# Kernel optimization log

Measured on AMD Instinct MI355X. Metric: run time of the kernel, lower is better.

Reference implementation:

```python
import jax, jax.numpy as jnp
import numpy as np

EPS_BN = 1e-5
HEADS = 4
K = 16

def _bn_eval(x, g, b, m, v):
    # eval-mode BatchNorm1d over the feature (last) axis
    return (x - m) * (g / jnp.sqrt(v + EPS_BN)) + b

def setup_inputs() -> dict:
    key = jax.random.key(0)
    ks = jax.random.split(key, 32)
    B, T, N, C = 8, 4, 2048, 11
    D = 64
    hd = D // HEADS
    s = 0.05
    rn = lambda k, shp: jax.random.normal(k, shp, jnp.float32) * s
    inp = {
        'x': jax.random.normal(ks[0], (B, T, N, C), jnp.float32),
        # PointEmbedding: Linear(11,32) + BN(32) + ReLU + Linear(32,64) + BN(64) + ReLU
        'emb_w1': rn(ks[1], (32, C)), 'emb_b1': rn(ks[2], (32,)),
        'bn1_g': jnp.ones((32,)), 'bn1_b': jnp.zeros((32,)),
        'bn1_m': rn(ks[3], (32,)), 'bn1_v': jnp.ones((32,)),
        'emb_w2': rn(ks[4], (D, 32)), 'emb_b2': rn(ks[5], (D,)),
        'bn2_g': jnp.ones((D,)), 'bn2_b': jnp.zeros((D,)),
        'bn2_m': rn(ks[6], (D,)), 'bn2_v': jnp.ones((D,)),
        # DenseGATLayer
        'gat_W': rn(ks[7], (D, D)),          # Linear(64,64,bias=False)
        'att': rn(ks[8], (HEADS, 2 * hd)),    # attention vector per head
        # TemporalCrossAttention
        'q_w': rn(ks[9], (D, D)), 'q_b': rn(ks[10], (D,)),
        'kv_w': rn(ks[11], (D, D)), 'kv_b': rn(ks[12], (D,)),
        # heads
        'lw1': rn(ks[13], (32, D)), 'lb1': rn(ks[14], (32,)),
        'lw2': rn(ks[15], (4, 32)), 'lb2': rn(ks[16], (4,)),
        'rw1': rn(ks[17], (32, D)), 'rb1': rn(ks[18], (32,)),
        'rw2': rn(ks[19], (4, 32)), 'rb2': rn(ks[20], (4,)),
    }
    return inp

def _forward(x, emb_w1, emb_b1, bn1_g, bn1_b, bn1_m, bn1_v,
             emb_w2, emb_b2, bn2_g, bn2_b, bn2_m, bn2_v,
             gat_W, att, q_w, q_b, kv_w, kv_b,
             lw1, lb1, lw2, lb2, rw1, rb1, rw2, rb2):
    B, T, N, C = x.shape
    D = gat_W.shape[0]
    hd = D // HEADS
    BT = B * T
    xf = x.reshape(BT, N, C)

    # ---- PointEmbedding (BN in eval mode) ----
    h = xf @ emb_w1.T + emb_b1
    h = jax.nn.relu(_bn_eval(h, bn1_g, bn1_b, bn1_m, bn1_v))
    h = h @ emb_w2.T + emb_b2
    h = jax.nn.relu(_bn_eval(h, bn2_g, bn2_b, bn2_m, bn2_v))  # [BT,N,D]

    # ---- DenseGATLayer ----
    pos = xf[:, :, :2]  # raw xy
    sq = jnp.sum(pos * pos, axis=-1)  # [BT,N]
    d2 = sq[:, :, None] + sq[:, None, :] - 2.0 * jnp.einsum('bnc,bmc->bnm', pos, pos)
    _, idx = jax.lax.top_k(-d2, K)  # k nearest (incl self), [BT,N,K]

    hw = (h @ gat_W.T).reshape(BT, N, HEADS, hd)  # [BT,N,H,hd]
    h_nb = jax.vmap(lambda hb, ib: hb[ib])(hw, idx)  # [BT,N,K,H,hd]

    att_self, att_nb = att[:, :hd], att[:, hd:]
    s_self = jnp.einsum('bnhd,hd->bnh', hw, att_self)       # [BT,N,H]
    s_nb = jnp.einsum('bnkhd,hd->bnkh', h_nb, att_nb)        # [BT,N,K,H]
    scores = jax.nn.leaky_relu(s_self[:, :, None, :] + s_nb, 0.2)
    alpha = jax.nn.softmax(scores, axis=2)                   # softmax over K
    out = jnp.einsum('bnkhd,bnkh->bnhd', h_nb, alpha).reshape(BT, N, D)
    h_sp = jax.nn.relu(out + h)  # [BT,N,D]

    # ---- TemporalCrossAttention ----
    ht = h_sp.reshape(B, T, N, D).transpose(0, 2, 1, 3)  # [B,N,T,D]
    Q = ht[:, :, -1, :] @ q_w.T + q_b                    # [B,N,D]
    KV = ht @ kv_w.T + kv_b                              # [B,N,T,D]
    sc = jnp.einsum('bnd,bntd->bnt', Q, KV) / jnp.sqrt(jnp.float32(D))
    w = jax.nn.softmax(sc, axis=-1)
    h_fused = jnp.einsum('bnt,bntd->bnd', w, KV)         # [B,N,D]

    # ---- heads ----
    ol = jax.nn.relu(h_fused @ lw1.T + lb1) @ lw2.T + lb2
    orr = jax.nn.relu(h_fused @ rw1.T + rb1) @ rw2.T + rb2
    lidar_mu, lidar_sigma = ol[:, :, :2], jax.nn.softplus(ol[:, :, 2:]) + 1e-6
    radar_mu, radar_sigma = orr[:, :, :2], jax.nn.softplus(orr[:, :, 2:]) + 1e-6
    return ((lidar_mu, lidar_sigma), (radar_mu, radar_sigma))

def reference(x, emb_w1, emb_b1, bn1_g, bn1_b, bn1_m, bn1_v,
              emb_w2, emb_b2, bn2_g, bn2_b, bn2_m, bn2_v,
              gat_W, att, q_w, q_b, kv_w, kv_b,
              lw1, lb1, lw2, lb2, rw1, rb1, rw2, rb2):
    return _forward(x, emb_w1, emb_b1, bn1_g, bn1_b, bn1_m, bn1_v,
                    emb_w2, emb_b2, bn2_g, bn2_b, bn2_m, bn2_v,
                    gat_W, att, q_w, q_b, kv_w, kv_b,
                    lw1, lb1, lw2, lb2, rw1, rb1, rw2, rb2)
```

## Files before the change

### kernel.cpp

```cpp
#include <hip/hip_runtime.h>
#include <math.h>

#define B_ 8
#define T_ 4
#define N_ 2048
#define C_ 11
#define D_ 64
#define H_ 4
#define HD_ 16
#define K_ 16
#define BT_ (B_*T_)

__device__ __forceinline__ float softplus_f(float x) {
    return fmaxf(x, 0.f) + log1pf(expf(-fabsf(x)));
}

__global__ __launch_bounds__(1024) void k_sort(const float* __restrict__ x,
    float2* __restrict__ sp2g, int* __restrict__ sidg, int* __restrict__ fail_cnt)
{
    __shared__ unsigned long long kvs[N_];
    __shared__ float lyy[N_];
    int t = threadIdx.x, bt = blockIdx.x;
    if (t == 0) fail_cnt[bt] = 0;
    const float* xb = x + (size_t)bt * N_ * C_;
    for (int m = t; m < N_; m += 1024) {
        float a = xb[m*C_], b = xb[m*C_+1];
        unsigned int bits = __float_as_uint(a);
        unsigned int u = (bits & 0x80000000u) ? ~bits : (bits | 0x80000000u);
        kvs[m] = ((unsigned long long)u << 11) | (unsigned)m;
        lyy[m] = b;
    }
    __syncthreads();
    for (int k = 2; k <= N_; k <<= 1) {
        for (int j = k >> 1; j > 0; j >>= 1) {
            int p = t;
            int i = ((p & ~(j-1)) << 1) | (p & (j-1));
            int l = i | j;
            unsigned long long a = kvs[i], b = kvs[l];
            bool asc = (i & k) == 0;
            if ((a > b) == asc) { kvs[i] = b; kvs[l] = a; }
            __syncthreads();
        }
    }
    float2* op = sp2g + (size_t)bt * N_;
    int*    oi = sidg + (size_t)bt * N_;
    for (int m = t; m < N_; m += 1024) {
        unsigned long long key = kvs[m];
        int id = (int)(key & 0x7FFull);
        unsigned int u = (unsigned int)(key >> 11);
        unsigned int bits = (u & 0x80000000u) ? (u & 0x7FFFFFFFu) : ~u;
        op[m] = make_float2(__uint_as_float(bits), lyy[id]);
        oi[m] = id;
    }
}

__global__ __launch_bounds__(256) void k_embed(
    const float* __restrict__ x,
    const float* __restrict__ w1, const float* __restrict__ b1,
    const float* __restrict__ g1, const float* __restrict__ bb1,
    const float* __restrict__ m1, const float* __restrict__ v1,
    const float* __restrict__ w2, const float* __restrict__ b2,
    const float* __restrict__ g2, const float* __restrict__ bb2,
    const float* __restrict__ m2, const float* __restrict__ v2,
    float* __restrict__ h)
{
    __shared__ float sw1[32*C_], sb1[32], sw2[D_*32], sb2[D_];
    int t = threadIdx.x;
    if (t < 32) {
        float s = g1[t] / sqrtf(v1[t] + 1e-5f);
        sb1[t] = (b1[t] - m1[t]) * s + bb1[t];
        for (int c = 0; c < C_; ++c) sw1[t*C_+c] = w1[t*C_+c] * s;
    } else if (t >= 64 && t < 128) {
        int j = t - 64;
        float s = g2[j] / sqrtf(v2[j] + 1e-5f);
        sb2[j] = (b2[j] - m2[j]) * s + bb2[j];
        int key = (j >> 4) & 3;
        for (int c = 0; c < 32; ++c)
            sw2[j*32 + ((((c>>2) ^ key) << 2) | (c & 3))] = w2[j*32+c] * s;
    }
    __syncthreads();

    int node = blockIdx.x * 64 + (t >> 2);
    int g = t & 3;
    const float* xp = x + (size_t)node * C_;
    float xin[C_];
    #pragma unroll
    for (int c = 0; c < C_; ++c) xin[c] = xp[c];

    float t1[32];
    #pragma unroll
    for (int j = 0; j < 32; ++j) {
        float a = sb1[j];
        #pragma unroll
        for (int c = 0; c < C_; ++c) a = fmaf(xin[c], sw1[j*C_+c], a);
        t1[j] = fmaxf(a, 0.f);
    }
    float4* hp4 = (float4*)(h + (size_t)node * D_ + g * 16);
    #pragma unroll
    for (int j4 = 0; j4 < 4; ++j4) {
        float o[4];
        #pragma unroll
        for (int u = 0; u < 4; ++u) {
            int j = g*16 + j4*4 + u;
            float a = sb2[j];
            #pragma unroll
            for (int c4 = 0; c4 < 8; ++c4) {
                float4 w4 = *(const float4*)(&sw2[j*32 + ((c4 ^ g) << 2)]);
                a = fmaf(t1[4*c4+0], w4.x, a);
                a = fmaf(t1[4*c4+1], w4.y, a);
                a = fmaf(t1[4*c4+2], w4.z, a);
                a = fmaf(t1[4*c4+3], w4.w, a);
            }
            o[u] = fmaxf(a, 0.f);
        }
        hp4[j4] = make_float4(o[0], o[1], o[2], o[3]);
    }
}

__global__ __launch_bounds__(256) void k_gatw(
    const float* __restrict__ h, const float* __restrict__ gw,
    const float* __restrict__ att,
    float* __restrict__ hw, float* __restrict__ ssf, float* __restrict__ snbf)
{
    __shared__ float sw[D_*D_];
    __shared__ float satA[2*H_*HD_];
    int t = threadIdx.x;
    for (int i = t; i < D_*D_; i += 256) {
        int r = i >> 6, c = i & 63;
        sw[r*64 + ((((c>>2) ^ ((r>>4)&3)) << 2) | (c & 3))] = gw[i];
    }
    if (t < 2*H_*HD_) satA[t] = att[t];
    __syncthreads();

    int node = blockIdx.x * 64 + (t >> 2);
    int hh = t & 3;
    const float* hp = h + (size_t)node * D_;
    float hin[D_];
    #pragma unroll
    for (int j = 0; j < D_; j += 4) {
        float4 v = *(const float4*)(hp + j);
        hin[j] = v.x; hin[j+1] = v.y; hin[j+2] = v.z; hin[j+3] = v.w;
    }
    float4* wp4 = (float4*)(hw + (size_t)node * D_ + hh * HD_);
    float ss = 0.f, sn = 0.f;
    #pragma unroll
    for (int q4 = 0; q4 < 4; ++q4) {
        float o[4];
        #pragma unroll
        for (int u = 0; u < 4; ++u) {
            const int jj = q4*4 + u;
            const int j = hh*HD_ + jj;
            float a = 0.f;
            #pragma unroll
            for (int c4 = 0; c4 < D_/4; ++c4) {
                float4 w4 = *(const float4*)(&sw[j*64 + ((c4 ^ hh) << 2)]);
                a = fmaf(hin[4*c4+0], w4.x, a);
                a = fmaf(hin[4*c4+1], w4.y, a);
                a = fmaf(hin[4*c4+2], w4.z, a);
                a = fmaf(hin[4*c4+3], w4.w, a);
            }
            o[u] = a;
            ss = fmaf(a, satA[hh*(2*HD_) + jj], ss);
            sn = fmaf(a, satA[hh*(2*HD_) + HD_ + jj], sn);
        }
        wp4[q4] = make_float4(o[0], o[1], o[2], o[3]);
    }
    ssf[(size_t)node * H_ + hh] = ss;
    snbf[(size_t)node * H_ + hh] = sn;
}

__global__ __launch_bounds__(256) void k_knn_b1(const float2* __restrict__ sp2g,
    const int* __restrict__ sidg, int* __restrict__ idx,
    int* __restrict__ fail_cnt, int* __restrict__ fail_lst)
{
    __shared__ float2 spw[640];
    __shared__ int sidw[640];
    __shared__ int scnt[64];
    const int bt    = blockIdx.x >> 5;
    const int qbase = (blockIdx.x & 31) << 6;
    const int base  = qbase - 288;
    const float2* pb = sp2g + (size_t)bt * N_;
    const int*    ib = sidg + (size_t)bt * N_;
    for (int L = threadIdx.x; L < 640; L += 256) {
        int r = base + L;
        if (r < 0 || r >= N_) { spw[L] = make_float2(1e18f, 0.f); sidw[L] = 0; }
        else { spw[L] = pb[r]; sidw[L] = ib[r]; }
    }
    if (threadIdx.x < 64) scnt[threadIdx.x] = 0;
    __syncthreads();

    const int q = threadIdx.x >> 2;
    const int g = threadIdx.x & 3;
    const int s = qbase + q;
    const int sLoc = q + 288;
    const float xs = spw[sLoc].x, ys = spw[sLoc].y;
    const float sqn = __fmaf_rn(xs, xs, __fmul_rn(ys, ys));

    float bd[K_];
    #pragma unroll
    for (int i = 0; i < K_; ++i) bd[i] = 3.402823466e38f;

    for (int i = 0; i < 8; ++i) {
        float d[16];
        #pragma unroll
        for (int j = 0; j < 16; ++j) {
            float2 p = spw[q + 32 + 64*i + 4*j + g];
            float sps = __fmaf_rn(p.x, p.x, __fmul_rn(p.y, p.y));
            float tt = __fmul_rn(xs, p.x);
            tt = __fmaf_rn(ys, p.y, tt);
            d[j] = __fmaf_rn(-2.f, tt, sps);
        }
        #pragma unroll
        for (int k = 2; k <= 16; k <<= 1) {
            #pragma unroll
            for (int jj = k >> 1; jj > 0; jj >>= 1) {
                #pragma unroll
                for (int ii = 0; ii < 16; ++ii) {
                    int ll = ii ^ jj;
                    if (ll > ii) {
                        float lo = fminf(d[ii], d[ll]);
                        float hi = fmaxf(d[ii], d[ll]);
                        if ((ii & k) == 0) { d[ii] = lo; d[ll] = hi; }
                        else               { d[ii] = hi; d[ll] = lo; }
                    }
                }
            }
        }
        #pragma unroll
        for (int ii = 0; ii < 16; ++ii) bd[ii] = fminf(bd[ii], d[15-ii]);
        #pragma unroll
        for (int jj = 8; jj > 0; jj >>= 1) {
            #pragma unroll
            for (int ii = 0; ii < 16; ++ii) {
                int ll = ii ^ jj;
                if (ll > ii) {
                    float lo = fminf(bd[ii], bd[ll]);
                    float hi = fmaxf(bd[ii], bd[ll]);
                    bd[ii] = lo; bd[ll] = hi;
                }
            }
        }
    }

    #pragma unroll
    for (int st = 1; st <= 2; st <<= 1) {
        float pr[K_];
        #pragma unroll
        for (int i = 0; i < K_; ++i) pr[i] = __shfl_xor(bd[K_-1-i], st, 64);
        #pragma unroll
        for (int i = 0; i < K_; ++i) bd[i] = fminf(bd[i], pr[i]);
        #pragma unroll
        for (int dd = 8; dd >= 1; dd >>= 1) {
            #pragma unroll
            for (int i = 0; i < K_; ++i) {
                if ((i & dd) == 0) {
                    float lo = fminf(bd[i], bd[i+dd]);
                    float hi = fmaxf(bd[i], bd[i+dd]);
                    bd[i] = lo; bd[i+dd] = hi;
                }
            }
        }
    }
    const float d15 = bd[K_-1];

    float d15s = d15 + sqn;
    float bound = d15s * 1.0001f + (sqn + 1.0f) * 1e-5f;
    bool leftOK = (s - 257 < 0);
    if (!leftOK) { float gp = xs - spw[q+31].x;  leftOK  = (gp*gp >= bound); }
    bool rightOK = (s + 256 > N_-1);
    if (!rightOK){ float gp = spw[q+544].x - xs; rightOK = (gp*gp >= bound); }
    if (!(leftOK && rightOK) && g == 0) {
        int fp = atomicAdd(&fail_cnt[bt], 1);
        fail_lst[bt*N_ + fp] = s;
    }

    int n = sidw[sLoc];
    int* op = idx + ((size_t)bt * N_ + n) * K_;
    for (int i = 0; i < 16; ++i) {
        float d[8];
        int Lb = q + 32 + 32*i + g;
        #pragma unroll
        for (int j = 0; j < 8; ++j) {
            float2 p = spw[Lb + 4*j];
            float sps = __fmaf_rn(p.x, p.x, __fmul_rn(p.y, p.y));
            float tt = __fmul_rn(xs, p.x);
            tt = __fmaf_rn(ys, p.y, tt);
            d[j] = __fmaf_rn(-2.f, tt, sps);
        }
        float dm0 = fminf(fminf(d[0],d[1]), fminf(d[2],d[3]));
        float dm1 = fminf(fminf(d[4],d[5]), fminf(d[6],d[7]));
        if (fminf(dm0, dm1) <= d15) {
            #pragma unroll
            for (int j = 0; j < 8; ++j) {
                if (d[j] <= d15) {
                    int c = atomicAdd(&scnt[q], 1);
                    if (c < K_) op[c] = sidw[Lb + 4*j];
                }
            }
        }
    }
}

__global__ __launch_bounds__(256) void k_knn_b2(const float2* __restrict__ sp2g,
    const int* __restrict__ sidg, const int* __restrict__ fail_cnt,
    const int* __restrict__ fail_lst, int* __restrict__ idx)
{
    const int bt    = blockIdx.x >> 7;
    const int chunk = blockIdx.x & 127;
    const int nf = fail_cnt[bt];
    if (chunk * 16 >= nf) return;

    __shared__ float2 sp[N_];
    __shared__ int sid[N_];
    __shared__ int scnt[16];
    const float2* pb = sp2g + (size_t)bt * N_;
    const int*    ib = sidg + (size_t)bt * N_;
    for (int m = threadIdx.x; m < N_; m += 256) { sp[m] = pb[m]; sid[m] = ib[m]; }
    if (threadIdx.x < 16) scnt[threadIdx.x] = 0;
    __syncthreads();

    const int q = threadIdx.x >> 4;
    const int g = threadIdx.x & 15;
    const bool active = (chunk*16 + q) < nf;
    const int s = active ? fail_lst[bt*N_ + chunk*16 + q] : 0;
    const float xs = sp[s].x, ys = sp[s].y;

    float bd[K_];
    #pragma unroll
    for (int i = 0; i < K_; ++i) bd[i] = 3.402823466e38f;

    for (int i = 0; i < 8; ++i) {
        float d[16];
        #pragma unroll
        for (int j = 0; j < 16; ++j) {
            float2 p = sp[256*i + 16*j + g];
            float sps = __fmaf_rn(p.x, p.x, __fmul_rn(p.y, p.y));
            float tt = __fmul_rn(xs, p.x);
            tt = __fmaf_rn(ys, p.y, tt);
            d[j] = __fmaf_rn(-2.f, tt, sps);
        }
        #pragma unroll
        for (int k = 2; k <= 16; k <<= 1) {
            #pragma unroll
            for (int jj = k >> 1; jj > 0; jj >>= 1) {
                #pragma unroll
                for (int ii = 0; ii < 16; ++ii) {
                    int ll = ii ^ jj;
                    if (ll > ii) {
                        float lo = fminf(d[ii], d[ll]);
                        float hi = fmaxf(d[ii], d[ll]);
                        if ((ii & k) == 0) { d[ii] = lo; d[ll] = hi; }
                        else               { d[ii] = hi; d[ll] = lo; }
                    }
                }
            }
        }
        #pragma unroll
        for (int ii = 0; ii < 16; ++ii) bd[ii] = fminf(bd[ii], d[15-ii]);
        #pragma unroll
        for (int jj = 8; jj > 0; jj >>= 1) {
            #pragma unroll
            for (int ii = 0; ii < 16; ++ii) {
                int ll = ii ^ jj;
                if (ll > ii) {
                    float lo = fminf(bd[ii], bd[ll]);
                    float hi = fmaxf(bd[ii], bd[ll]);
                    bd[ii] = lo; bd[ll] = hi;
                }
            }
        }
    }

    #pragma unroll
    for (int st = 1; st <= 8; st <<= 1) {
        float pr[K_];
        #pragma unroll
        for (int i = 0; i < K_; ++i) pr[i] = __shfl_xor(bd[K_-1-i], st, 64);
        #pragma unroll
        for (int i = 0; i < K_; ++i) bd[i] = fminf(bd[i], pr[i]);
        #pragma unroll
        for (int dd = 8; dd >= 1; dd >>= 1) {
            #pragma unroll
            for (int i = 0; i < K_; ++i) {
                if ((i & dd) == 0) {
                    float lo = fminf(bd[i], bd[i+dd]);
                    float hi = fmaxf(bd[i], bd[i+dd]);
                    bd[i] = lo; bd[i+dd] = hi;
                }
            }
        }
    }
    const float d15 = bd[K_-1];

    int n = sid[s];
    int* op = idx + ((size_t)bt * N_ + n) * K_;
    for (int i = 0; i < 16; ++i) {
        float d[8];
        #pragma unroll
        for (int j = 0; j < 8; ++j) {
            float2 p = sp[128*i + 16*j + g];
            float sps = __fmaf_rn(p.x, p.x, __fmul_rn(p.y, p.y));
            float tt = __fmul_rn(xs, p.x);
            tt = __fmaf_rn(ys, p.y, tt);
            d[j] = __fmaf_rn(-2.f, tt, sps);
        }
        float dm0 = fminf(fminf(d[0],d[1]), fminf(d[2],d[3]));
        float dm1 = fminf(fminf(d[4],d[5]), fminf(d[6],d[7]));
        if (active && fminf(dm0, dm1) <= d15) {
            #pragma unroll
            for (int j = 0; j < 8; ++j) {
                if (d[j] <= d15) {
                    int c = atomicAdd(&scnt[q], 1);
                    if (c < K_) op[c] = sid[128*i + 16*j + g];
                }
            }
        }
    }
}

__global__ __launch_bounds__(256, 4) void k_gat(
    const float* __restrict__ hw, const float* __restrict__ ssf,
    const float* __restrict__ snbf,
    const int* __restrict__ idx,
    float* __restrict__ h )
{
    const int t = threadIdx.x;
    const int xcd   = blockIdx.x & 7;
    const int local = blockIdx.x >> 3;
    const int btl   = local >> 5;
    const int chunk = local & 31;
    const int bt    = xcd * 4 + btl;
    const int node  = bt * N_ + chunk * 64 + (t >> 2);
    const int hh    = t & 3;

    const int* ip = idx + (size_t)node * K_;
    float ssv = ssf[(size_t)node*H_ + hh];
    const float* hwb = hw + ((size_t)bt * N_) * D_;
    const float* snb = snbf + ((size_t)bt * N_) * H_;

    int nb[K_];
    #pragma unroll
    for (int k = 0; k < K_; ++k) nb[k] = ip[k];

    float sc[K_];
    float mx = -3.402823466e38f;
    #pragma unroll
    for (int k = 0; k < K_; ++k) {
        float s = ssv + snb[(size_t)nb[k]*H_ + hh];
        s = (s >= 0.f) ? s : 0.2f * s;
        sc[k] = s;
        mx = fmaxf(mx, s);
    }
    float den = 0.f;
    #pragma unroll
    for (int k = 0; k < K_; ++k) { sc[k] = __expf(sc[k] - mx); den += sc[k]; }
    float inv = 1.f / den;

    float acc[HD_];
    #pragma unroll
    for (int i = 0; i < HD_; ++i) acc[i] = 0.f;
    #pragma unroll
    for (int k = 0; k < K_; ++k) {
        float al = sc[k] * inv;
        const float* vp = hwb + (size_t)nb[k]*D_ + hh*HD_;
        #pragma unroll
        for (int i = 0; i < HD_; i += 4) {
            float4 v = *(const float4*)(vp + i);
            acc[i]   = fmaf(v.x, al, acc[i]);
            acc[i+1] = fmaf(v.y, al, acc[i+1]);
            acc[i+2] = fmaf(v.z, al, acc[i+2]);
            acc[i+3] = fmaf(v.w, al, acc[i+3]);
        }
    }
    float4* hp4 = (float4*)(h + (size_t)node*D_ + hh*HD_);
    #pragma unroll
    for (int i4 = 0; i4 < 4; ++i4) {
        float4 old = hp4[i4];
        hp4[i4] = make_float4(fmaxf(acc[4*i4+0] + old.x, 0.f),
                              fmaxf(acc[4*i4+1] + old.y, 0.f),
                              fmaxf(acc[4*i4+2] + old.z, 0.f),
                              fmaxf(acc[4*i4+3] + old.w, 0.f));
    }
}

__global__ __launch_bounds__(256) void k_qkv(
    const float* __restrict__ hsp,
    const float* __restrict__ qw, const float* __restrict__ qb,
    const float* __restrict__ kw, const float* __restrict__ kb,
    float* __restrict__ q, float* __restrict__ kv)
{
    __shared__ float s_qw[D_*D_], s_kw[D_*D_], s_qb[D_], s_kb[D_];
    int t = threadIdx.x;
    for (int i = t; i < D_*D_; i += 256) {
        int r = i >> 6, c = i & 63;
        int p = r*64 + ((((c>>2) ^ ((r>>4)&3)) << 2) | (c & 3));
        s_qw[p] = qw[i]; s_kw[p] = kw[i];
    }
    if (t < D_) { s_qb[t] = qb[t]; s_kb[t] = kb[t]; }
    __syncthreads();

    int r = blockIdx.x * 64 + (t >> 2);
    int g = t & 3;
    const float* in; float* outp; const float* W; const float* bb;
    if (r < BT_*N_) {
        int bt = r >> 11; int n = r & (N_-1);
        int b = bt >> 2, tt = bt & 3;
        in = hsp + (size_t)r * D_;
        outp = kv + (((size_t)(b*N_ + n))*T_ + tt) * D_;
        W = s_kw; bb = s_kb;
    } else {
        int rr = r - BT_*N_;
        int b = rr >> 11, n = rr & (N_-1);
        in = hsp + ((size_t)(b*T_ + (T_-1))*N_ + n) * D_;
        outp = q + (size_t)rr * D_;
        W = s_qw; bb = s_qb;
    }
    float xin[D_];
    #pragma unroll
    for (int j = 0; j < D_; j += 4) {
        float4 v = *(const float4*)(in + j);
        xin[j] = v.x; xin[j+1] = v.y; xin[j+2] = v.z; xin[j+3] = v.w;
    }
    float4* outp4 = (float4*)(outp + g * 16);
    #pragma unroll
    for (int j4 = 0; j4 < 4; ++j4) {
        float o[4];
        #pragma unroll
        for (int u = 0; u < 4; ++u) {
            int j = g*16 + j4*4 + u;
            float a = bb[j];
            #pragma unroll
            for (int c4 = 0; c4 < D_/4; ++c4) {
                float4 w4 = *(const float4*)(&W[j*64 + ((c4 ^ g) << 2)]);
                a = fmaf(xin[4*c4+0], w4.x, a);
                a = fmaf(xin[4*c4+1], w4.y, a);
                a = fmaf(xin[4*c4+2], w4.z, a);
                a = fmaf(xin[4*c4+3], w4.w, a);
            }
            o[u] = a;
        }
        outp4[j4] = make_float4(o[0], o[1], o[2], o[3]);
    }
}

__global__ __launch_bounds__(64) void k_head(
    const float* __restrict__ q, const float* __restrict__ kv,
    const float* __restrict__ lw1, const float* __restrict__ lb1,
    const float* __restrict__ lw2, const float* __restrict__ lb2,
    const float* __restrict__ rw1, const float* __restrict__ rb1,
    const float* __restrict__ rw2, const float* __restrict__ rb2,
    float* __restrict__ out)
{
    __shared__ float sl1[32*D_], sr1[32*D_], sl2[4*32], sr2[4*32];
    __shared__ float slb1[32], srb1[32], slb2[4], srb2[4];
    int t = threadIdx.x;
    for (int i = t; i < 32*D_; i += 64) { sl1[i] = lw1[i]; sr1[i] = rw1[i]; }
    for (int i = t; i < 128; i += 64)   { sl2[i] = lw2[i]; sr2[i] = rw2[i]; }
    if (t < 32) { slb1[t] = lb1[t]; srb1[t] = rb1[t]; }
    if (t < 4)  { slb2[t] = lb2[t]; srb2[t] = rb2[t]; }
    __syncthreads();

    int rn = blockIdx.x * 64 + t;
    const float* qp = q + (size_t)rn * D_;
    const float* kp = kv + (size_t)rn * T_ * D_;

    float qv[D_];
    #pragma unroll
    for (int j = 0; j < D_; j += 4) {
        float4 v = *(const float4*)(qp + j);
        qv[j] = v.x; qv[j+1] = v.y; qv[j+2] = v.z; qv[j+3] = v.w;
    }
    float scv[T_];
    #pragma unroll
    for (int tt = 0; tt < T_; ++tt) {
        float a = 0.f;
        const float4* kr = (const float4*)(kp + tt*D_);
        #pragma unroll
        for (int c4 = 0; c4 < D_/4; ++c4) {
            float4 v = kr[c4];
            a = fmaf(qv[4*c4+0], v.x, a);
            a = fmaf(qv[4*c4+1], v.y, a);
            a = fmaf(qv[4*c4+2], v.z, a);
            a = fmaf(qv[4*c4+3], v.w, a);
        }
        scv[tt] = a * 0.125f;
    }
    float mx = fmaxf(fmaxf(scv[0], scv[1]), fmaxf(scv[2], scv[3]));
    float wsum = 0.f;
    #pragma unroll
    for (int tt = 0; tt < T_; ++tt) { scv[tt] = expf(scv[tt] - mx); wsum += scv[tt]; }
    float winv = 1.f / wsum;

    float hf[D_];
    #pragma unroll
    for (int j = 0; j < D_; ++j) hf[j] = 0.f;
    #pragma unroll
    for (int tt = 0; tt < T_; ++tt) {
        float w = scv[tt] * winv;
        const float4* kr = (const float4*)(kp + tt*D_);
        #pragma unroll
        for (int c4 = 0; c4 < D_/4; ++c4) {
            float4 v = kr[c4];
            hf[4*c4+0] = fmaf(v.x, w, hf[4*c4+0]);
            hf[4*c4+1] = fmaf(v.y, w, hf[4*c4+1]);
            hf[4*c4+2] = fmaf(v.z, w, hf[4*c4+2]);
            hf[4*c4+3] = fmaf(v.w, w, hf[4*c4+3]);
        }
    }
    float ol0 = slb2[0], ol1 = slb2[1], ol2 = slb2[2], ol3 = slb2[3];
    #pragma unroll 2
    for (int j = 0; j < 32; ++j) {
        float a = slb1[j];
        const float4* wr = (const float4*)(&sl1[j*D_]);
        #pragma unroll
        for (int c4 = 0; c4 < D_/4; ++c4) {
            float4 v = wr[c4];
            a = fmaf(hf[4*c4+0], v.x, a);
            a = fmaf(hf[4*c4+1], v.y, a);
            a = fmaf(hf[4*c4+2], v.z, a);
            a = fmaf(hf[4*c4+3], v.w, a);
        }
        a = fmaxf(a, 0.f);
        ol0 = fmaf(a, sl2[0*32+j], ol0);
        ol1 = fmaf(a, sl2[1*32+j], ol1);
        ol2 = fmaf(a, sl2[2*32+j], ol2);
        ol3 = fmaf(a, sl2[3*32+j], ol3);
    }
    float or0 = srb2[0], or1 = srb2[1], or2 = srb2[2], or3 = srb2[3];
    #pragma unroll 2
    for (int j = 0; j < 32; ++j) {
        float a = srb1[j];
        const float4* wr = (const float4*)(&sr1[j*D_]);
        #pragma unroll
        for (int c4 = 0; c4 < D_/4; ++c4) {
            float4 v = wr[c4];
            a = fmaf(hf[4*c4+0], v.x, a);
            a = fmaf(hf[4*c4+1], v.y, a);
            a = fmaf(hf[4*c4+2], v.z, a);
            a = fmaf(hf[4*c4+3], v.w, a);
        }
        a = fmaxf(a, 0.f);
        or0 = fmaf(a, sr2[0*32+j], or0);
        or1 = fmaf(a, sr2[1*32+j], or1);
        or2 = fmaf(a, sr2[2*32+j], or2);
        or3 = fmaf(a, sr2[3*32+j], or3);
    }
    const int NB = B_ * N_;
    out[0*2*NB + rn*2 + 0] = ol0;
    out[0*2*NB + rn*2 + 1] = ol1;
    out[1*2*NB + rn*2 + 0] = softplus_f(ol2) + 1e-6f;
    out[1*2*NB + rn*2 + 1] = softplus_f(ol3) + 1e-6f;
    out[2*2*NB + rn*2 + 0] = or0;
    out[2*2*NB + rn*2 + 1] = or1;
    out[3*2*NB + rn*2 + 0] = softplus_f(or2) + 1e-6f;
    out[3*2*NB + rn*2 + 1] = softplus_f(or3) + 1e-6f;
}

extern "C" void kernel_launch(void* const* d_in, const int* in_sizes, int n_in,
                              void* d_out, int out_size, void* d_ws, size_t ws_size,
                              hipStream_t stream)
{
    const float* x   = (const float*)d_in[0];
    const float* ew1 = (const float*)d_in[1];
    const float* eb1 = (const float*)d_in[2];
    const float* g1  = (const float*)d_in[3];
    const float* bb1 = (const float*)d_in[4];
    const float* m1  = (const float*)d_in[5];
    const float* v1  = (const float*)d_in[6];
    const float* ew2 = (const float*)d_in[7];
    const float* eb2 = (const float*)d_in[8];
    const float* g2  = (const float*)d_in[9];
    const float* bb2 = (const float*)d_in[10];
    const float* m2  = (const float*)d_in[11];
    const float* v2  = (const float*)d_in[12];
    const float* gw  = (const float*)d_in[13];
    const float* att = (const float*)d_in[14];
    const float* qw  = (const float*)d_in[15];
    const float* qb  = (const float*)d_in[16];
    const float* kw  = (const float*)d_in[17];
    const float* kb  = (const float*)d_in[18];
    const float* lw1 = (const float*)d_in[19];
    const float* lb1 = (const float*)d_in[20];
    const float* lw2 = (const float*)d_in[21];
    const float* lb2 = (const float*)d_in[22];
    const float* rw1 = (const float*)d_in[23];
    const float* rb1 = (const float*)d_in[24];
    const float* rw2 = (const float*)d_in[25];
    const float* rb2 = (const float*)d_in[26];
    float* out = (float*)d_out;

    const size_t NTOT = (size_t)BT_*N_;
    float* h    = (float*)d_ws;
    float* hw   = h   + NTOT*D_;
    float* kvb  = hw  + NTOT*D_;
    float* ssf  = kvb + NTOT*D_;
    float* snbf = ssf + NTOT*H_;
    int*   idx  = (int*)(snbf + NTOT*H_);
    float* q    = (float*)(idx + NTOT*K_);
    float2* sp2g = (float2*)(q + (size_t)B_*N_*D_);
    int*   sidg = (int*)((float*)sp2g + 2*NTOT);
    int*   fail_cnt = sidg + NTOT;
    int*   fail_lst = fail_cnt + 32;

    k_sort<<<BT_, 1024, 0, stream>>>(x, sp2g, sidg, fail_cnt);
    k_embed<<<BT_*N_/64, 256, 0, stream>>>(x, ew1, eb1, g1, bb1, m1, v1,
                                           ew2, eb2, g2, bb2, m2, v2, h);
    k_gatw<<<BT_*N_/64, 256, 0, stream>>>(h, gw, att, hw, ssf, snbf);
    k_knn_b1<<<BT_*(N_/64), 256, 0, stream>>>(sp2g, sidg, idx, fail_cnt, fail_lst);
    k_knn_b2<<<BT_*128, 256, 0, stream>>>(sp2g, sidg, fail_cnt, fail_lst, idx);
    k_gat<<<(BT_*N_*H_)/256, 256, 0, stream>>>(hw, ssf, snbf, idx, h);
    k_qkv<<<(BT_*N_ + B_*N_)/64, 256, 0, stream>>>(h, qw, qb, kw, kb, q, kvb);
    k_head<<<(B_*N_)/64, 64, 0, stream>>>(q, kvb, lw1, lb1, lw2, lb2,
                                          rw1, rb1, rw2, rb2, out);
}
```

Before: 216.8 us.

## Merge independent kernels into block-partitioned launches to overlap sort/embed and gatw/knn

Result: faster. 210.6 us (median of 3 runs) (-2.8%).

```diff
diff --git a/kernel.cpp b/kernel.cpp
--- a/kernel.cpp
+++ b/kernel.cpp
@@ -15,46 +15,7 @@
     return fmaxf(x, 0.f) + log1pf(expf(-fabsf(x)));
 }
 
-__global__ __launch_bounds__(1024) void k_sort(const float* __restrict__ x,
-    float2* __restrict__ sp2g, int* __restrict__ sidg, int* __restrict__ fail_cnt)
-{
-    __shared__ unsigned long long kvs[N_];
-    __shared__ float lyy[N_];
-    int t = threadIdx.x, bt = blockIdx.x;
-    if (t == 0) fail_cnt[bt] = 0;
-    const float* xb = x + (size_t)bt * N_ * C_;
-    for (int m = t; m < N_; m += 1024) {
-        float a = xb[m*C_], b = xb[m*C_+1];
-        unsigned int bits = __float_as_uint(a);
-        unsigned int u = (bits & 0x80000000u) ? ~bits : (bits | 0x80000000u);
-        kvs[m] = ((unsigned long long)u << 11) | (unsigned)m;
-        lyy[m] = b;
-    }
-    __syncthreads();
-    for (int k = 2; k <= N_; k <<= 1) {
-        for (int j = k >> 1; j > 0; j >>= 1) {
-            int p = t;
-            int i = ((p & ~(j-1)) << 1) | (p & (j-1));
-            int l = i | j;
-            unsigned long long a = kvs[i], b = kvs[l];
-            bool asc = (i & k) == 0;
-            if ((a > b) == asc) { kvs[i] = b; kvs[l] = a; }
-            __syncthreads();
-        }
-    }
-    float2* op = sp2g + (size_t)bt * N_;
-    int*    oi = sidg + (size_t)bt * N_;
-    for (int m = t; m < N_; m += 1024) {
-        unsigned long long key = kvs[m];
-        int id = (int)(key & 0x7FFull);
-        unsigned int u = (unsigned int)(key >> 11);
-        unsigned int bits = (u & 0x80000000u) ? (u & 0x7FFFFFFFu) : ~u;
-        op[m] = make_float2(__uint_as_float(bits), lyy[id]);
-        oi[m] = id;
-    }
-}
-
-__global__ __launch_bounds__(256) void k_embed(
+__global__ __launch_bounds__(1024) void k_root(
     const float* __restrict__ x,
     const float* __restrict__ w1, const float* __restrict__ b1,
     const float* __restrict__ g1, const float* __restrict__ bb1,
@@ -62,135 +23,182 @@
     const float* __restrict__ w2, const float* __restrict__ b2,
     const float* __restrict__ g2, const float* __restrict__ bb2,
     const float* __restrict__ m2, const float* __restrict__ v2,
-    float* __restrict__ h)
+    float* __restrict__ h,
+    float2* __restrict__ sp2g, int* __restrict__ sidg, int* __restrict__ fail_cnt)
 {
-    __shared__ float sw1[32*C_], sb1[32], sw2[D_*32], sb2[D_];
+    __shared__ unsigned long long smemU[3072];
     int t = threadIdx.x;
-    if (t < 32) {
-        float s = g1[t] / sqrtf(v1[t] + 1e-5f);
-        sb1[t] = (b1[t] - m1[t]) * s + bb1[t];
-        for (int c = 0; c < C_; ++c) sw1[t*C_+c] = w1[t*C_+c] * s;
-    } else if (t >= 64 && t < 128) {
-        int j = t - 64;
-        float s = g2[j] / sqrtf(v2[j] + 1e-5f);
-        sb2[j] = (b2[j] - m2[j]) * s + bb2[j];
-        int key = (j >> 4) & 3;
-        for (int c = 0; c < 32; ++c)
-            sw2[j*32 + ((((c>>2) ^ key) << 2) | (c & 3))] = w2[j*32+c] * s;
-    }
-    __syncthreads();
-
-    int node = blockIdx.x * 64 + (t >> 2);
-    int g = t & 3;
-    const float* xp = x + (size_t)node * C_;
-    float xin[C_];
-    #pragma unroll
-    for (int c = 0; c < C_; ++c) xin[c] = xp[c];
-
-    float t1[32];
-    #pragma unroll
-    for (int j = 0; j < 32; ++j) {
-        float a = sb1[j];
-        #pragma unroll
-        for (int c = 0; c < C_; ++c) a = fmaf(xin[c], sw1[j*C_+c], a);
-        t1[j] = fmaxf(a, 0.f);
-    }
-    float4* hp4 = (float4*)(h + (size_t)node * D_ + g * 16);
-    #pragma unroll
-    for (int j4 = 0; j4 < 4; ++j4) {
-        float o[4];
-        #pragma unroll
-        for (int u = 0; u < 4; ++u) {
-            int j = g*16 + j4*4 + u;
-            float a = sb2[j];
-            #pragma unroll
-            for (int c4 = 0; c4 < 8; ++c4) {
-                float4 w4 = *(const float4*)(&sw2[j*32 + ((c4 ^ g) << 2)]);
-                a = fmaf(t1[4*c4+0], w4.x, a);
-                a = fmaf(t1[4*c4+1], w4.y, a);
-                a = fmaf(t1[4*c4+2], w4.z, a);
-                a = fmaf(t1[4*c4+3], w4.w, a);
-            }
-            o[u] = fmaxf(a, 0.f);
-        }
-        hp4[j4] = make_float4(o[0], o[1], o[2], o[3]);
+
+    if (blockIdx.x < BT_) {
+        unsigned long long* kvs = smemU;
+        float* lyy = (float*)(smemU + 2048);
+        int bt = blockIdx.x;
+        if (t == 0) fail_cnt[bt] = 0;
+        const float* xb = x + (size_t)bt * N_ * C_;
+        for (int m = t; m < N_; m += 1024) {
+            float a = xb[m*C_], b = xb[m*C_+1];
+            unsigned int bits = __float_as_uint(a);
+            unsigned int u = (bits & 0x80000000u) ? ~bits : (bits | 0x80000000u);
+            kvs[m] = ((unsigned long long)u << 11) | (unsigned)m;
+            lyy[m] = b;
+        }
+        __syncthreads();
+        for (int k = 2; k <= N_; k <<= 1) {
+            for (int j = k >> 1; j > 0; j >>= 1) {
+                int p = t;
+                int i = ((p & ~(j-1)) << 1) | (p & (j-1));
+                int l = i | j;
+                unsigned long long a = kvs[i], b = kvs[l];
+                bool asc = (i & k) == 0;
+                if ((a > b) == asc) { kvs[i] = b; kvs[l] = a; }
+                __syncthreads();
+            }
+        }
+        float2* op = sp2g + (size_t)bt * N_;
+        int*    oi = sidg + (size_t)bt * N_;
+        for (int m = t; m < N_; m += 1024) {
+            unsigned long long key = kvs[m];
+            int id = (int)(key & 0x7FFull);
+            unsigned int u = (unsigned int)(key >> 11);
+            unsigned int bits = (u & 0x80000000u) ? (u & 0x7FFFFFFFu) : ~u;
+            op[m] = make_float2(__uint_as_float(bits), lyy[id]);
+            oi[m] = id;
+        }
+    } else {
+        float* fs  = (float*)smemU;
+        float* sw1 = fs;
+        float* sb1 = fs + 352;
+        float* sw2 = fs + 384;
+        float* sb2 = fs + 2432;
+        if (t < 32) {
+            float s = g1[t] / sqrtf(v1[t] + 1e-5f);
+            sb1[t] = (b1[t] - m1[t]) * s + bb1[t];
+            for (int c = 0; c < C_; ++c) sw1[t*C_+c] = w1[t*C_+c] * s;
+        } else if (t >= 64 && t < 128) {
+            int j = t - 64;
+            float s = g2[j] / sqrtf(v2[j] + 1e-5f);
+            sb2[j] = (b2[j] - m2[j]) * s + bb2[j];
+            int key = (j >> 4) & 3;
+            for (int c = 0; c < 32; ++c)
+                sw2[j*32 + ((((c>>2) ^ key) << 2) | (c & 3))] = w2[j*32+c] * s;
+        }
+        __syncthreads();
+
+        int node = (blockIdx.x - BT_) * 256 + (t >> 2);
+        int g = t & 3;
+        const float* xp = x + (size_t)node * C_;
+        float xin[C_];
+        #pragma unroll
+        for (int c = 0; c < C_; ++c) xin[c] = xp[c];
+
+        float t1[32];
+        #pragma unroll
+        for (int j = 0; j < 32; ++j) {
+            float a = sb1[j];
+            #pragma unroll
+            for (int c = 0; c < C_; ++c) a = fmaf(xin[c], sw1[j*C_+c], a);
+            t1[j] = fmaxf(a, 0.f);
+        }
+        float4* hp4 = (float4*)(h + (size_t)node * D_ + g * 16);
+        #pragma unroll
+        for (int j4 = 0; j4 < 4; ++j4) {
+            float o[4];
+            #pragma unroll
+            for (int u = 0; u < 4; ++u) {
+                int j = g*16 + j4*4 + u;
+                float a = sb2[j];
+                #pragma unroll
+                for (int c4 = 0; c4 < 8; ++c4) {
+                    float4 w4 = *(const float4*)(&sw2[j*32 + ((c4 ^ g) << 2)]);
+                    a = fmaf(t1[4*c4+0], w4.x, a);
+                    a = fmaf(t1[4*c4+1], w4.y, a);
+                    a = fmaf(t1[4*c4+2], w4.z, a);
+                    a = fmaf(t1[4*c4+3], w4.w, a);
+                }
+                o[u] = fmaxf(a, 0.f);
+            }
+            hp4[j4] = make_float4(o[0], o[1], o[2], o[3]);
+        }
     }
 }
 
-__global__ __launch_bounds__(256) void k_gatw(
+__global__ __launch_bounds__(256) void k_gatw_b1(
     const float* __restrict__ h, const float* __restrict__ gw,
     const float* __restrict__ att,
-    float* __restrict__ hw, float* __restrict__ ssf, float* __restrict__ snbf)
+    float* __restrict__ hw, float* __restrict__ ssf, float* __restrict__ snbf,
+    const float2* __restrict__ sp2g, const int* __restrict__ sidg,
+    int* __restrict__ idx, int* __restrict__ fail_cnt, int* __restrict__ fail_lst)
 {
-    __shared__ float sw[D_*D_];
-    __shared__ float satA[2*H_*HD_];
+    __shared__ float4 smemQ[1088];
     int t = threadIdx.x;
-    for (int i = t; i < D_*D_; i += 256) {
-        int r = i >> 6, c = i & 63;
-        sw[r*64 + ((((c>>2) ^ ((r>>4)&3)) << 2) | (c & 3))] = gw[i];
-    }
-    if (t < 2*H_*HD_) satA[t] = att[t];
-    __syncthreads();
-
-    int node = blockIdx.x * 64 + (t >> 2);
-    int hh = t & 3;
-    const float* hp = h + (size_t)node * D_;
-    float hin[D_];
-    #pragma unroll
-    for (int j = 0; j < D_; j += 4) {
-        float4 v = *(const float4*)(hp + j);
-        hin[j] = v.x; hin[j+1] = v.y; hin[j+2] = v.z; hin[j+3] = v.w;
-    }
-    float4* wp4 = (float4*)(hw + (size_t)node * D_ + hh * HD_);
-    float ss = 0.f, sn = 0.f;
-    #pragma unroll
-    for (int q4 = 0; q4 < 4; ++q4) {
-        float o[4];
-        #pragma unroll
-        for (int u = 0; u < 4; ++u) {
-            const int jj = q4*4 + u;
-            const int j = hh*HD_ + jj;
-            float a = 0.f;
-            #pragma unroll
-            for (int c4 = 0; c4 < D_/4; ++c4) {
-                float4 w4 = *(const float4*)(&sw[j*64 + ((c4 ^ hh) << 2)]);
-                a = fmaf(hin[4*c4+0], w4.x, a);
-                a = fmaf(hin[4*c4+1], w4.y, a);
-                a = fmaf(hin[4*c4+2], w4.z, a);
-                a = fmaf(hin[4*c4+3], w4.w, a);
-            }
-            o[u] = a;
-            ss = fmaf(a, satA[hh*(2*HD_) + jj], ss);
-            sn = fmaf(a, satA[hh*(2*HD_) + HD_ + jj], sn);
-        }
-        wp4[q4] = make_float4(o[0], o[1], o[2], o[3]);
-    }
-    ssf[(size_t)node * H_ + hh] = ss;
-    snbf[(size_t)node * H_ + hh] = sn;
-}
-
-__global__ __launch_bounds__(256) void k_knn_b1(const float2* __restrict__ sp2g,
-    const int* __restrict__ sidg, int* __restrict__ idx,
-    int* __restrict__ fail_cnt, int* __restrict__ fail_lst)
-{
-    __shared__ float2 spw[640];
-    __shared__ int sidw[640];
-    __shared__ int scnt[64];
-    const int bt    = blockIdx.x >> 5;
-    const int qbase = (blockIdx.x & 31) << 6;
+
+    if (blockIdx.x < BT_*N_/64) {
+        float* sw   = (float*)smemQ;
+        float* satA = sw + 4096;
+        for (int i = t; i < D_*D_; i += 256) {
+            int r = i >> 6, c = i & 63;
+            sw[r*64 + ((((c>>2) ^ ((r>>4)&3)) << 2) | (c & 3))] = gw[i];
+        }
+        if (t < 2*H_*HD_) satA[t] = att[t];
+        __syncthreads();
+
+        int node = blockIdx.x * 64 + (t >> 2);
+        int hh = t & 3;
+        const float* hp = h + (size_t)node * D_;
+        float hin[D_];
+        #pragma unroll
+        for (int j = 0; j < D_; j += 4) {
+            float4 v = *(const float4*)(hp + j);
+            hin[j] = v.x; hin[j+1] = v.y; hin[j+2] = v.z; hin[j+3] = v.w;
+        }
+        float4* wp4 = (float4*)(hw + (size_t)node * D_ + hh * HD_);
+        float ss = 0.f, sn = 0.f;
+        #pragma unroll
+        for (int q4 = 0; q4 < 4; ++q4) {
+            float o[4];
+            #pragma unroll
+            for (int u = 0; u < 4; ++u) {
+                const int jj = q4*4 + u;
+                const int j = hh*HD_ + jj;
+                float a = 0.f;
+                #pragma unroll
+                for (int c4 = 0; c4 < D_/4; ++c4) {
+                    float4 w4 = *(const float4*)(&sw[j*64 + ((c4 ^ hh) << 2)]);
+                    a = fmaf(hin[4*c4+0], w4.x, a);
+                    a = fmaf(hin[4*c4+1], w4.y, a);
+                    a = fmaf(hin[4*c4+2], w4.z, a);
+                    a = fmaf(hin[4*c4+3], w4.w, a);
+                }
+                o[u] = a;
+                ss = fmaf(a, satA[hh*(2*HD_) + jj], ss);
+                sn = fmaf(a, satA[hh*(2*HD_) + HD_ + jj], sn);
+            }
+            wp4[q4] = make_float4(o[0], o[1], o[2], o[3]);
+        }
+        ssf[(size_t)node * H_ + hh] = ss;
+        snbf[(size_t)node * H_ + hh] = sn;
+        return;
+    }
+
+    float2* spw = (float2*)smemQ;
+    int* sidw   = (int*)((float*)smemQ + 1280);
+    int* scnt   = sidw + 640;
+    const int bid   = blockIdx.x - BT_*N_/64;
+    const int bt    = bid >> 5;
+    const int qbase = (bid & 31) << 6;
     const int base  = qbase - 288;
     const float2* pb = sp2g + (size_t)bt * N_;
     const int*    ib = sidg + (size_t)bt * N_;
-    for (int L = threadIdx.x; L < 640; L += 256) {
+    for (int L = t; L < 640; L += 256) {
         int r = base + L;
         if (r < 0 || r >= N_) { spw[L] = make_float2(1e18f, 0.f); sidw[L] = 0; }
         else { spw[L] = pb[r]; sidw[L] = ib[r]; }
     }
-    if (threadIdx.x < 64) scnt[threadIdx.x] = 0;
+    if (t < 64) scnt[t] = 0;
     __syncthreads();
 
-    const int q = threadIdx.x >> 2;
-    const int g = threadIdx.x & 3;
+    const int q = t >> 2;
+    const int g = t & 3;
     const int s = qbase + q;
     const int sLoc = q + 288;
     const float xs = spw[sLoc].x, ys = spw[sLoc].y;
@@ -702,11 +710,11 @@
     int*   fail_cnt = sidg + NTOT;
     int*   fail_lst = fail_cnt + 32;
 
-    k_sort<<<BT_, 1024, 0, stream>>>(x, sp2g, sidg, fail_cnt);
-    k_embed<<<BT_*N_/64, 256, 0, stream>>>(x, ew1, eb1, g1, bb1, m1, v1,
-                                           ew2, eb2, g2, bb2, m2, v2, h);
-    k_gatw<<<BT_*N_/64, 256, 0, stream>>>(h, gw, att, hw, ssf, snbf);
-    k_knn_b1<<<BT_*(N_/64), 256, 0, stream>>>(sp2g, sidg, idx, fail_cnt, fail_lst);
+    k_root<<<BT_ + BT_*N_/256, 1024, 0, stream>>>(x, ew1, eb1, g1, bb1, m1, v1,
+                                                  ew2, eb2, g2, bb2, m2, v2,
+                                                  h, sp2g, sidg, fail_cnt);
+    k_gatw_b1<<<BT_*N_/64 + BT_*(N_/64), 256, 0, stream>>>(
+        h, gw, att, hw, ssf, snbf, sp2g, sidg, idx, fail_cnt, fail_lst);
     k_knn_b2<<<BT_*128, 256, 0, stream>>>(sp2g, sidg, fail_cnt, fail_lst, idx);
     k_gat<<<(BT_*N_*H_)/256, 256, 0, stream>>>(hw, ssf, snbf, idx, h);
     k_qkv<<<(BT_*N_ + B_*N_)/64, 256, 0, stream>>>(h, qw, qb, kw, kb, q, kvb);
```
